# Kernel tuning notes

Measured on AMD Instinct MI355X. Metric: run time of the kernel, lower is better.

## Reference

```python
import jax, jax.numpy as jnp
import numpy as np
from jax.scipy.special import gammaln

L, R, W0, W1, B = 100, 3, 5, 20, 50


def mish(x):
    return x * jnp.tanh(jax.nn.softplus(x))


def conv1d(x, w, b):
    y = jax.lax.conv_general_dilated(x, w, (1,), 'VALID', dimension_numbers=('NCH', 'OIH', 'NCH'))
    return y + b[None, :, None]


def maxpool2(x):
    n = (x.shape[-1] // 2) * 2
    return x[..., :n].reshape(x.shape[0], x.shape[1], -1, 2).max(-1)


def dir_lp(x, alpha):
    # Dirichlet(alpha) log-prob over last dim, capped at 3.0 as in pwm_pr_lp/gamma_pr_lp
    K = x.shape[-1]
    lp = ((alpha - 1.0) * jnp.log(x)).sum(-1) + gammaln(K * alpha) - K * gammaln(alpha)
    return jnp.minimum(3.0, lp)


def binom_lp(n, k):
    # Binomial(n, 0.5) log pmf
    return gammaln(n + 1.0) - gammaln(k + 1.0) - gammaln(n - k + 1.0) + n * jnp.log(0.5)


def dlog_lp(a, b, mean, s, x):
    # DiscreteLogistic on [a,b]; log_prob evaluated at shifted value x (true value v = x + a)
    v = x + a
    up = jnp.where(v >= b, 1.0, jax.nn.sigmoid((v + 0.5 - mean) / s))
    lo = jnp.where(v <= a, 0.0, jax.nn.sigmoid((v - 0.5 - mean) / s))
    return jnp.log(up - lo + 1e-12)


def elbo(pwm_logits, wn_W1, wn_b1, wn_W2, wn_b2, wn_W3, wn_b3,
         gn_c1W, gn_c1b, gn_c2W, gn_c2b, gn_l1W, gn_l1b, gn_l2W, gn_l2b,
         zn_c1W, zn_c1b, zn_c2W, zn_c2b, zn_clsW, zn_clsb, zn_delW, zn_delb, X):
    pwm = jax.nn.softmax(pwm_logits, -1)              # [R,W1,4] PWM probabilities
    pwm_log = jnp.log(pwm)
    log_prior = dir_lp(pwm, 0.2).sum()
    # w guide net (Dropout inactive at eval)
    h = mish(wn_W1[0] + wn_b1)
    h = mish(h @ wn_W2 + wn_b2)
    ww = jax.nn.sigmoid(h @ wn_W3 + wn_b3)            # [R]
    mean = ww * (W1 - W0) + W0
    # cartesian product of floor/ceil per motif (torch.cartesian_prod: first var slowest)
    bits = (jnp.arange(8)[:, None] >> jnp.arange(2, -1, -1)[None, :]) & 1
    w2f = jnp.where(bits == 1, jnp.ceil(mean)[None, :], jnp.floor(mean)[None, :])  # [8,R]
    w_lp = dlog_lp(float(W0), float(W1), mean[None, :], 0.05, w2f - W0)            # [8,R]
    w_prob = jnp.exp(w_lp).T                                                        # [R,8]
    log_prior = log_prior + jnp.dot(w_prob.prod(0), binom_lp(float(W1 - W0), w2f).sum(1))
    log_guide = jnp.dot(w_prob.prod(0), w_lp.sum(1))
    # S[b,j,p,k] = log pwm[j,k,X[b,p+k]] -- replaces diag_embed + conv1d + log
    pidx = jnp.clip(jnp.arange(L)[:, None] + jnp.arange(W1)[None, :], 0, L - 1)
    Xoh = jax.nn.one_hot(X[:, pidx], 4, dtype=pwm.dtype)                            # [B,L,W1,4]
    S = jnp.einsum('bpkc,jkc->bjpk', Xoh, pwm_log)                                  # [B,R,L,W1]
    q = jnp.arange(L)
    kk = jnp.arange(W1)
    log_X = jnp.float32(0.0)
    for i_w in range(2 ** R):
        w = w2f[i_w].astype(jnp.int32)                                              # [R]
        kmask = (kk[None, :] < w[:, None]).astype(S.dtype)                          # [R,W1]
        ymid = (S * kmask[None, :, None, :]).sum(-1) / w.astype(S.dtype)[None, :, None]
        left = (w - 1) // 2
        valid = (q[None, :] >= left[:, None]) & (q[None, :] <= left[:, None] + (L - w)[:, None])
        src = jnp.clip(q[None, :] - left[:, None], 0, L - 1)
        ysh = jnp.take_along_axis(ymid, jnp.broadcast_to(src[None], ymid.shape), axis=2)
        y = jnp.where(valid[None], ysh, 0.0)                                        # [B,R,L]
        # gamma_net
        g = maxpool2(mish(conv1d(y, gn_c1W, gn_c1b)))
        g = maxpool2(mish(conv1d(g, gn_c2W, gn_c2b))).reshape(B, -1)                # [B,22]
        g = mish(g @ gn_l1W + gn_l1b)
        gamma = jax.nn.softmax(g @ gn_l2W + gn_l2b, -1)                             # [B,R]
        log_prior = log_prior + w_prob[:, i_w].prod() * dir_lp(gamma, 0.2).sum()
        for I in range(R):
            wI = w[I]
            I_pr = gamma[:, I]
            # z_net
            z = maxpool2(mish(conv1d(y[:, I:I + 1, :], zn_c1W, zn_c1b)))
            z = maxpool2(mish(conv1d(z, zn_c2W, zn_c2b))).reshape(B, -1)            # [B,176]
            Z_cls = z @ zn_clsW + zn_clsb                                           # [B,9]
            Z_del = jax.nn.sigmoid(z @ zn_delW + zn_delb)                           # [B,10]
            ind = jnp.argmax(Z_cls, 1) + 1
            gap = (99 - W1) / 10.0
            Z_m = (ind.astype(S.dtype) + Z_del[jnp.arange(B), ind]) * gap
            Z2 = jnp.stack([jnp.floor(Z_m), jnp.ceil(Z_m)], 0).astype(jnp.int32)    # [2,B]
            Z2f = Z2.astype(S.dtype)
            Z_lp = dlog_lp(0.0, 99.0, Z_m[None], 0.05, Z2f)
            Z_prob = jnp.exp(Z_lp)
            log_prior = log_prior + (w_prob[I, i_w] * Z_prob * I_pr[None] * binom_lp(float(L - W1 - 1), Z2f)).sum()
            log_guide = log_guide + (w_prob[I, i_w] * Z_prob * I_pr[None] * Z_lp).sum()
            # log_X: vectorized per-sample gather of pwm[I, k, X[i, Z+k]] for k < wI
            pos = jnp.clip(Z2[:, :, None] + kk[None, None, :], 0, L - 1)            # [2,B,W1]
            Xs = X[jnp.arange(B)[None, :, None], pos]                               # [2,B,W1]
            val = pwm_log[I][kk[None, None, :], Xs]                                 # [2,B,W1]
            lpv = (val * (kk[None, None, :] < wI)).sum(-1)                          # [2,B]
            log_X = log_X + w_prob[I, i_w] * (Z_prob * I_pr[None] * lpv).sum()
    return -log_X - log_prior + log_guide


def setup_inputs() -> dict:
    key = jax.random.key(0)
    ks = jax.random.split(key, 32)
    def n(i, shape, s=0.1):
        return (jax.random.normal(ks[i], shape) * s).astype(jnp.float32)
    return {
        'pwm_logits': n(0, (R, W1, 4), 0.5),
        'wn_W1': n(1, (1, 16)), 'wn_b1': n(2, (16,)),
        'wn_W2': n(3, (16, 16)), 'wn_b2': n(4, (16,)),
        'wn_W3': n(5, (16, 3), 0.01), 'wn_b3': n(6, (3,), 0.01),
        'gn_c1W': n(7, (16, 3, 5)), 'gn_c1b': n(8, (16,)),
        'gn_c2W': n(9, (1, 16, 5)), 'gn_c2b': n(10, (1,)),
        'gn_l1W': n(11, (22, 16)), 'gn_l1b': n(12, (16,)),
        'gn_l2W': n(13, (16, 3)), 'gn_l2b': n(14, (3,)),
        'zn_c1W': n(15, (16, 1, 5)), 'zn_c1b': n(16, (16,)),
        'zn_c2W': n(17, (8, 16, 5)), 'zn_c2b': n(18, (8,)),
        'zn_clsW': n(19, (176, 9)), 'zn_clsb': n(20, (9,)),
        'zn_delW': n(21, (176, 10)), 'zn_delb': n(22, (10,)),
        'X': jax.random.randint(ks[23], (B, L), 0, 4, dtype=jnp.int32),
    }


def reference(pwm_logits, wn_W1, wn_b1, wn_W2, wn_b2, wn_W3, wn_b3,
              gn_c1W, gn_c1b, gn_c2W, gn_c2b, gn_l1W, gn_l1b, gn_l2W, gn_l2b,
              zn_c1W, zn_c1b, zn_c2W, zn_c2b, zn_clsW, zn_clsb, zn_delW, zn_delb, X):
    return elbo(pwm_logits, wn_W1, wn_b1, wn_W2, wn_b2, wn_W3, wn_b3,
                gn_c1W, gn_c1b, gn_c2W, gn_c2b, gn_l1W, gn_l1b, gn_l2W, gn_l2b,
                zn_c1W, zn_c1b, zn_c2W, zn_c2b, zn_clsW, zn_clsb, zn_delW, zn_delb, X)
```

## Files before the change

kernel.cpp:

```cpp
#include <hip/hip_runtime.h>
#include <math.h>

#define LN2F 0.69314718055994530942f

#define WS_PWMLOG 0
#define WS_PJT    240
#define WS_WPROD  246
#define WS_BASEP  254
#define WS_BASEG  255
#define WS_WVF    256
#define WS_Y      272
#define WS_GAMMA  30272
#define WS_ZT     31472

__device__ __forceinline__ float sigm(float x){ return 1.0f/(1.0f+expf(-x)); }
__device__ __forceinline__ float mishf(float x){
    float sp = fmaxf(x,0.0f) + log1pf(expf(-fabsf(x)));
    return x * tanhf(sp);
}

__global__ void kA(const float* __restrict__ pwm_logits,
                   const float* __restrict__ wn_W1, const float* __restrict__ wn_b1,
                   const float* __restrict__ wn_W2, const float* __restrict__ wn_b2,
                   const float* __restrict__ wn_W3, const float* __restrict__ wn_b3,
                   float* __restrict__ ws)
{
    __shared__ float red[64];
    __shared__ float h1[16], h2s[16];
    int tid = threadIdx.x;
    float C4 = lgammaf(0.8f) - 4.0f*lgammaf(0.2f);
    float part = 0.0f;
    if (tid < 60) {
        const float* l = pwm_logits + tid*4;
        float m = fmaxf(fmaxf(l[0],l[1]),fmaxf(l[2],l[3]));
        float se = expf(l[0]-m)+expf(l[1]-m)+expf(l[2]-m)+expf(l[3]-m);
        float ls = logf(se);
        float dsum = 0.0f;
        for(int c=0;c<4;c++){ float pl = l[c]-m-ls; ws[WS_PWMLOG+tid*4+c]=pl; dsum+=pl; }
        float lp = -0.8f*dsum + C4;
        part = fminf(3.0f, lp);
    }
    red[tid]=part;
    __syncthreads();
    for(int s=32;s>0;s>>=1){ if(tid<s) red[tid]+=red[tid+s]; __syncthreads(); }

    if (tid<16) h1[tid] = mishf(wn_W1[tid]+wn_b1[tid]);
    __syncthreads();
    if (tid<16){
        float acc = wn_b2[tid];
        for(int i=0;i<16;i++) acc += h1[i]*wn_W2[i*16+tid];
        h2s[tid]=mishf(acc);
    }
    __syncthreads();
    if (tid==0){
        float mean[3];
        for(int o=0;o<3;o++){
            float acc=wn_b3[o];
            for(int i=0;i<16;i++) acc += h2s[i]*wn_W3[i*3+o];
            mean[o] = sigm(acc)*15.0f + 5.0f;
        }
        float pjt[3][2], wlp[3][2], bin[3][2];
        for(int j=0;j<3;j++){
            for(int t=0;t<2;t++){
                float wv = t ? ceilf(mean[j]) : floorf(mean[j]);
                float up = (wv>=20.0f)?1.0f:sigm((wv+0.5f-mean[j])/0.05f);
                float lo = (wv<=5.0f)?0.0f:sigm((wv-0.5f-mean[j])/0.05f);
                wlp[j][t] = logf(up-lo+1e-12f);
                pjt[j][t] = expf(wlp[j][t]);
                bin[j][t] = lgammaf(16.0f)-lgammaf(wv+1.0f)-lgammaf(16.0f-wv)+15.0f*(-LN2F);
                ws[WS_PJT+j*2+t]=pjt[j][t];
                ws[WS_WVF+j*2+t]=wv;
            }
        }
        float bp = red[0];
        float bg = 0.0f;
        for(int i=0;i<8;i++){
            int b0=(i>>2)&1, b1=(i>>1)&1, b2=i&1;
            float wp = pjt[0][b0]*pjt[1][b1]*pjt[2][b2];
            ws[WS_WPROD+i]=wp;
            bp += wp*(bin[0][b0]+bin[1][b1]+bin[2][b2]);
            bg += wp*(wlp[0][b0]+wlp[1][b1]+wlp[2][b2]);
        }
        ws[WS_BASEP]=bp;
        ws[WS_BASEG]=bg;
    }
}

__global__ void kB(const int* __restrict__ X, float* __restrict__ ws)
{
    int jt = blockIdx.x, b = blockIdx.y;
    int j = jt>>1;
    __shared__ int   xs[100];
    __shared__ float plj[80];
    int tid=threadIdx.x;
    if (tid<100) xs[tid]=X[b*100+tid];
    if (tid<80)  plj[tid]=ws[WS_PWMLOG+j*80+tid];
    __syncthreads();
    if (tid<100){
        int w = (int)ws[WS_WVF+jt];
        int left=(w-1)>>1;
        float yv=0.0f;
        if (tid>=left && tid<=left+100-w){
            int src=tid-left;
            float s=0.0f;
            for(int k=0;k<w;k++){
                int p=src+k; if(p>99)p=99;
                s+=plj[k*4+xs[p]];
            }
            yv=s/(float)w;
        }
        ws[WS_Y+(jt*50+b)*100+tid]=yv;
    }
}

__global__ void kC(const float* __restrict__ c1W, const float* __restrict__ c1b,
                   const float* __restrict__ c2W, const float* __restrict__ c2b,
                   const float* __restrict__ l1W, const float* __restrict__ l1b,
                   const float* __restrict__ l2W, const float* __restrict__ l2b,
                   float* __restrict__ ws)
{
    int iw=blockIdx.x, b=blockIdx.y, tid=threadIdx.x;
    __shared__ float yc[3][100];
    __shared__ float cw1[240];
    __shared__ float hp[16][48];
    __shared__ float c2o[44];
    __shared__ float g22[22];
    __shared__ float h16[16];
    for(int i=tid;i<300;i+=256){
        int j=i/100, q=i%100;
        int t=(iw>>(2-j))&1;
        yc[j][q]=ws[WS_Y+((j*2+t)*50+b)*100+q];
    }
    for(int i=tid;i<240;i+=256) cw1[i]=c1W[i];
    __syncthreads();
    for(int idx=tid; idx<768; idx+=256){
        int o=idx/48, p2=idx%48;
        float m=-1e30f;
        const float* wr=&cw1[o*15];
        for(int d=0;d<2;d++){
            int p=2*p2+d;
            float acc=c1b[o];
            for(int i=0;i<3;i++)
                for(int k=0;k<5;k++) acc += yc[i][p+k]*wr[i*5+k];
            m=fmaxf(m, mishf(acc));
        }
        hp[o][p2]=m;
    }
    __syncthreads();
    if (tid<44){
        float acc=c2b[0];
        for(int i=0;i<16;i++)
            for(int k=0;k<5;k++) acc+=hp[i][tid+k]*c2W[i*5+k];
        c2o[tid]=mishf(acc);
    }
    __syncthreads();
    if (tid<22) g22[tid]=fmaxf(c2o[2*tid],c2o[2*tid+1]);
    __syncthreads();
    if (tid<16){
        float acc=l1b[tid];
        for(int i=0;i<22;i++) acc+=g22[i]*l1W[i*16+tid];
        h16[tid]=mishf(acc);
    }
    __syncthreads();
    if (tid==0){
        float o3[3]; float m=-1e30f;
        for(int o=0;o<3;o++){
            float acc=l2b[o];
            for(int i=0;i<16;i++) acc+=h16[i]*l2W[i*3+o];
            o3[o]=acc; m=fmaxf(m,acc);
        }
        float se=0.0f; for(int o=0;o<3;o++){o3[o]=expf(o3[o]-m); se+=o3[o];}
        for(int o=0;o<3;o++) ws[WS_GAMMA+(iw*50+b)*3+o]=o3[o]/se;
    }
}

__global__ void kD(const int* __restrict__ X,
                   const float* __restrict__ c1W, const float* __restrict__ c1b,
                   const float* __restrict__ c2W, const float* __restrict__ c2b,
                   const float* __restrict__ clsW, const float* __restrict__ clsb,
                   const float* __restrict__ delW, const float* __restrict__ delb,
                   float* __restrict__ ws)
{
    int It=blockIdx.x, b=blockIdx.y, tid=threadIdx.x;
    int I=It>>1;
    __shared__ float y1[100];
    __shared__ int   xs[100];
    __shared__ float plI[80];
    __shared__ float zw1[80];
    __shared__ float zw2[640];
    __shared__ float hp[16][48];
    __shared__ float c2o[8][44];
    __shared__ float z[176];
    __shared__ float cls[9], del[10];
    if (tid<100){ y1[tid]=ws[WS_Y+(It*50+b)*100+tid]; xs[tid]=X[b*100+tid]; }
    if (tid>=128 && tid<208) { plI[tid-128]=ws[WS_PWMLOG+I*80+(tid-128)]; zw1[tid-128]=c1W[tid-128]; }
    for(int i=tid;i<640;i+=256) zw2[i]=c2W[i];
    __syncthreads();
    for(int idx=tid; idx<768; idx+=256){
        int o=idx/48, p2=idx%48;
        float m=-1e30f;
        for(int d=0;d<2;d++){
            int p=2*p2+d;
            float acc=c1b[o];
            for(int k=0;k<5;k++) acc+=y1[p+k]*zw1[o*5+k];
            m=fmaxf(m, mishf(acc));
        }
        hp[o][p2]=m;
    }
    __syncthreads();
    for(int idx=tid; idx<352; idx+=256){
        int o=idx/44, p=idx%44;
        float acc=c2b[o];
        for(int i=0;i<16;i++)
            for(int k=0;k<5;k++) acc+=hp[i][p+k]*zw2[(o*16+i)*5+k];
        c2o[o][p]=mishf(acc);
    }
    __syncthreads();
    if (tid<176){
        int o=tid/22, q=tid%22;
        z[tid]=fmaxf(c2o[o][2*q],c2o[o][2*q+1]);
    }
    __syncthreads();
    if (tid<9){
        float acc=clsb[tid];
        for(int m2=0;m2<176;m2++) acc+=z[m2]*clsW[m2*9+tid];
        cls[tid]=acc;
    }
    if (tid>=64 && tid<74){
        int n=tid-64;
        float acc=delb[n];
        for(int m2=0;m2<176;m2++) acc+=z[m2]*delW[m2*10+n];
        del[n]=sigm(acc);
    }
    __syncthreads();
    if (tid==0){
        int ind=0; float best=cls[0];
        for(int n=1;n<9;n++) if(cls[n]>best){best=cls[n];ind=n;}
        ind+=1;
        float Zm=((float)ind+del[ind])*7.9f;
        int wI=(int)ws[WS_WVF+It];
        float r0=0.0f,r1=0.0f,r2=0.0f;
        for(int s=0;s<2;s++){
            float zf = s? ceilf(Zm):floorf(Zm);
            float up = (zf>=99.0f)?1.0f:sigm((zf+0.5f-Zm)/0.05f);
            float lo = (zf<=0.0f)?0.0f:sigm((zf-0.5f-Zm)/0.05f);
            float zlp = logf(up-lo+1e-12f);
            float zp  = expf(zlp);
            float bin = lgammaf(80.0f)-lgammaf(zf+1.0f)-lgammaf(80.0f-zf)+79.0f*(-LN2F);
            int zi=(int)zf;
            float lpv=0.0f;
            for(int k=0;k<wI;k++){
                int p=zi+k; if(p<0)p=0; if(p>99)p=99;
                lpv+=plI[k*4+xs[p]];
            }
            r0+=zp*bin; r1+=zp*zlp; r2+=zp*lpv;
        }
        ws[WS_ZT+      It*50+b]=r0;
        ws[WS_ZT+300 + It*50+b]=r1;
        ws[WS_ZT+600 + It*50+b]=r2;
    }
}

__global__ void kE(const float* __restrict__ ws, float* __restrict__ out)
{
    int tid=threadIdx.x;
    __shared__ float sa[256], sb[256], sc[256];
    float C3 = lgammaf(0.6f) - 3.0f*lgammaf(0.2f);
    float pp=0.0f, pg=0.0f, px=0.0f;
    for(int idx=tid; idx<400; idx+=256){
        int iw=idx/50, b=idx%50;
        const float* g=&ws[WS_GAMMA+(iw*50+b)*3];
        float lp=-0.8f*(logf(g[0])+logf(g[1])+logf(g[2]))+C3;
        lp=fminf(3.0f,lp);
        pp += ws[WS_WPROD+iw]*lp;
    }
    for(int idx=tid; idx<300; idx+=256){
        int It=idx/50, b=idx%50;
        int I=It>>1, t=It&1;
        float gs=0.0f;
        for(int iw=0;iw<8;iw++)
            if(((iw>>(2-I))&1)==t) gs+=ws[WS_GAMMA+(iw*50+b)*3+I];
        float G=ws[WS_PJT+It]*gs;
        pp += G*ws[WS_ZT+idx];
        pg += G*ws[WS_ZT+300+idx];
        px += G*ws[WS_ZT+600+idx];
    }
    sa[tid]=pp; sb[tid]=pg; sc[tid]=px;
    __syncthreads();
    for(int s=128;s>0;s>>=1){
        if(tid<s){sa[tid]+=sa[tid+s];sb[tid]+=sb[tid+s];sc[tid]+=sc[tid+s];}
        __syncthreads();
    }
    if(tid==0){
        float log_prior=ws[WS_BASEP]+sa[0];
        float log_guide=ws[WS_BASEG]+sb[0];
        float log_X=sc[0];
        out[0] = -log_X - log_prior + log_guide;
    }
}

extern "C" void kernel_launch(void* const* d_in, const int* in_sizes, int n_in,
                              void* d_out, int out_size, void* d_ws, size_t ws_size,
                              hipStream_t stream)
{
    const float* pwm_logits=(const float*)d_in[0];
    const float* wn_W1 =(const float*)d_in[1];
    const float* wn_b1 =(const float*)d_in[2];
    const float* wn_W2 =(const float*)d_in[3];
    const float* wn_b2 =(const float*)d_in[4];
    const float* wn_W3 =(const float*)d_in[5];
    const float* wn_b3 =(const float*)d_in[6];
    const float* gn_c1W=(const float*)d_in[7];
    const float* gn_c1b=(const float*)d_in[8];
    const float* gn_c2W=(const float*)d_in[9];
    const float* gn_c2b=(const float*)d_in[10];
    const float* gn_l1W=(const float*)d_in[11];
    const float* gn_l1b=(const float*)d_in[12];
    const float* gn_l2W=(const float*)d_in[13];
    const float* gn_l2b=(const float*)d_in[14];
    const float* zn_c1W=(const float*)d_in[15];
    const float* zn_c1b=(const float*)d_in[16];
    const float* zn_c2W=(const float*)d_in[17];
    const float* zn_c2b=(const float*)d_in[18];
    const float* zn_clsW=(const float*)d_in[19];
    const float* zn_clsb=(const float*)d_in[20];
    const float* zn_delW=(const float*)d_in[21];
    const float* zn_delb=(const float*)d_in[22];
    const int*   X     =(const int*)d_in[23];
    float* ws =(float*)d_ws;
    float* out=(float*)d_out;

    hipLaunchKernelGGL(kA, dim3(1),      dim3(64),  0, stream,
                       pwm_logits, wn_W1, wn_b1, wn_W2, wn_b2, wn_W3, wn_b3, ws);
    hipLaunchKernelGGL(kB, dim3(6,50),   dim3(128), 0, stream, X, ws);
    hipLaunchKernelGGL(kC, dim3(8,50),   dim3(256), 0, stream,
                       gn_c1W, gn_c1b, gn_c2W, gn_c2b, gn_l1W, gn_l1b, gn_l2W, gn_l2b, ws);
    hipLaunchKernelGGL(kD, dim3(6,50),   dim3(256), 0, stream,
                       X, zn_c1W, zn_c1b, zn_c2W, zn_c2b, zn_clsW, zn_clsb, zn_delW, zn_delb, ws);
    hipLaunchKernelGGL(kE, dim3(1),      dim3(256), 0, stream, ws, out);
}
```

Measured before the change: 143.6 us.

## Fuse five kernels into two by recomputing small shared prelude per block

Merges the PWM/width-net, sliding-window score, gamma-net and z-net kernels into one 700-block kernel. Each block recomputes the PWM log-softmax, the width net and its own window-score rows in shared memory, and the finalize kernel recomputes the prior terms itself. This removes three launches and the global round trips through workspace, in exchange for redundant tiny computations in every block. Mish is also rewritten with a single exp and an algebraic tanh(softplus) form instead of log1p plus tanh.

```diff
diff --git a/kernel.cpp b/kernel.cpp
--- a/kernel.cpp
+++ b/kernel.cpp
@@ -3,276 +3,279 @@
 
 #define LN2F 0.69314718055994530942f
 
-#define WS_PWMLOG 0
-#define WS_PJT    240
-#define WS_WPROD  246
-#define WS_BASEP  254
-#define WS_BASEG  255
-#define WS_WVF    256
-#define WS_Y      272
-#define WS_GAMMA  30272
-#define WS_ZT     31472
+#define WS_GAMMA 0
+#define WS_ZT    1200
 
 __device__ __forceinline__ float sigm(float x){ return 1.0f/(1.0f+expf(-x)); }
 __device__ __forceinline__ float mishf(float x){
-    float sp = fmaxf(x,0.0f) + log1pf(expf(-fabsf(x)));
-    return x * tanhf(sp);
+    if (x >= 30.0f) return x;
+    float w = expf(x);
+    float u = 1.0f + w; u *= u;
+    return x * (u - 1.0f) / (u + 1.0f);
 }
 
-__global__ void kA(const float* __restrict__ pwm_logits,
-                   const float* __restrict__ wn_W1, const float* __restrict__ wn_b1,
-                   const float* __restrict__ wn_W2, const float* __restrict__ wn_b2,
-                   const float* __restrict__ wn_W3, const float* __restrict__ wn_b3,
-                   float* __restrict__ ws)
+__global__ __launch_bounds__(256) void kMain(
+    const float* __restrict__ pwm_logits,
+    const float* __restrict__ wn_W1, const float* __restrict__ wn_b1,
+    const float* __restrict__ wn_W2, const float* __restrict__ wn_b2,
+    const float* __restrict__ wn_W3, const float* __restrict__ wn_b3,
+    const float* __restrict__ gc1W, const float* __restrict__ gc1b,
+    const float* __restrict__ gc2W, const float* __restrict__ gc2b,
+    const float* __restrict__ gl1W, const float* __restrict__ gl1b,
+    const float* __restrict__ gl2W, const float* __restrict__ gl2b,
+    const float* __restrict__ zc1W, const float* __restrict__ zc1b,
+    const float* __restrict__ zc2W, const float* __restrict__ zc2b,
+    const float* __restrict__ zclsW, const float* __restrict__ zclsb,
+    const float* __restrict__ zdelW, const float* __restrict__ zdelb,
+    const int* __restrict__ X, float* __restrict__ ws)
 {
-    __shared__ float red[64];
-    __shared__ float h1[16], h2s[16];
-    int tid = threadIdx.x;
-    float C4 = lgammaf(0.8f) - 4.0f*lgammaf(0.2f);
-    float part = 0.0f;
-    if (tid < 60) {
-        const float* l = pwm_logits + tid*4;
-        float m = fmaxf(fmaxf(l[0],l[1]),fmaxf(l[2],l[3]));
-        float se = expf(l[0]-m)+expf(l[1]-m)+expf(l[2]-m)+expf(l[3]-m);
-        float ls = logf(se);
-        float dsum = 0.0f;
-        for(int c=0;c<4;c++){ float pl = l[c]-m-ls; ws[WS_PWMLOG+tid*4+c]=pl; dsum+=pl; }
-        float lp = -0.8f*dsum + C4;
-        part = fminf(3.0f, lp);
-    }
-    red[tid]=part;
-    __syncthreads();
-    for(int s=32;s>0;s>>=1){ if(tid<s) red[tid]+=red[tid+s]; __syncthreads(); }
-
-    if (tid<16) h1[tid] = mishf(wn_W1[tid]+wn_b1[tid]);
-    __syncthreads();
-    if (tid<16){
-        float acc = wn_b2[tid];
-        for(int i=0;i<16;i++) acc += h1[i]*wn_W2[i*16+tid];
-        h2s[tid]=mishf(acc);
-    }
-    __syncthreads();
-    if (tid==0){
-        float mean[3];
-        for(int o=0;o<3;o++){
-            float acc=wn_b3[o];
-            for(int i=0;i<16;i++) acc += h2s[i]*wn_W3[i*3+o];
-            mean[o] = sigm(acc)*15.0f + 5.0f;
-        }
-        float pjt[3][2], wlp[3][2], bin[3][2];
-        for(int j=0;j<3;j++){
-            for(int t=0;t<2;t++){
-                float wv = t ? ceilf(mean[j]) : floorf(mean[j]);
-                float up = (wv>=20.0f)?1.0f:sigm((wv+0.5f-mean[j])/0.05f);
-                float lo = (wv<=5.0f)?0.0f:sigm((wv-0.5f-mean[j])/0.05f);
-                wlp[j][t] = logf(up-lo+1e-12f);
-                pjt[j][t] = expf(wlp[j][t]);
-                bin[j][t] = lgammaf(16.0f)-lgammaf(wv+1.0f)-lgammaf(16.0f-wv)+15.0f*(-LN2F);
-                ws[WS_PJT+j*2+t]=pjt[j][t];
-                ws[WS_WVF+j*2+t]=wv;
-            }
-        }
-        float bp = red[0];
-        float bg = 0.0f;
-        for(int i=0;i<8;i++){
-            int b0=(i>>2)&1, b1=(i>>1)&1, b2=i&1;
-            float wp = pjt[0][b0]*pjt[1][b1]*pjt[2][b2];
-            ws[WS_WPROD+i]=wp;
-            bp += wp*(bin[0][b0]+bin[1][b1]+bin[2][b2]);
-            bg += wp*(wlp[0][b0]+wlp[1][b1]+wlp[2][b2]);
-        }
-        ws[WS_BASEP]=bp;
-        ws[WS_BASEG]=bg;
-    }
-}
-
-__global__ void kB(const int* __restrict__ X, float* __restrict__ ws)
-{
-    int jt = blockIdx.x, b = blockIdx.y;
-    int j = jt>>1;
+    int tid=threadIdx.x, bid=blockIdx.x;
+    bool isC = bid < 400;
+    int iw=0, b, It=0, I=0;
+    if(isC){ iw=bid%8; b=bid/8; }
+    else   { int idx=bid-400; It=idx%6; b=idx/6; I=It>>1; }
+
+    __shared__ float pl[240];
     __shared__ int   xs[100];
-    __shared__ float plj[80];
-    int tid=threadIdx.x;
-    if (tid<100) xs[tid]=X[b*100+tid];
-    if (tid<80)  plj[tid]=ws[WS_PWMLOG+j*80+tid];
-    __syncthreads();
-    if (tid<100){
-        int w = (int)ws[WS_WVF+jt];
-        int left=(w-1)>>1;
-        float yv=0.0f;
-        if (tid>=left && tid<=left+100-w){
-            int src=tid-left;
-            float s=0.0f;
-            for(int k=0;k<w;k++){
-                int p=src+k; if(p>99)p=99;
-                s+=plj[k*4+xs[p]];
-            }
-            yv=s/(float)w;
-        }
-        ws[WS_Y+(jt*50+b)*100+tid]=yv;
-    }
-}
-
-__global__ void kC(const float* __restrict__ c1W, const float* __restrict__ c1b,
-                   const float* __restrict__ c2W, const float* __restrict__ c2b,
-                   const float* __restrict__ l1W, const float* __restrict__ l1b,
-                   const float* __restrict__ l2W, const float* __restrict__ l2b,
-                   float* __restrict__ ws)
-{
-    int iw=blockIdx.x, b=blockIdx.y, tid=threadIdx.x;
-    __shared__ float yc[3][100];
-    __shared__ float cw1[240];
-    __shared__ float hp[16][48];
-    __shared__ float c2o[44];
-    __shared__ float g22[22];
-    __shared__ float h16[16];
-    for(int i=tid;i<300;i+=256){
-        int j=i/100, q=i%100;
-        int t=(iw>>(2-j))&1;
-        yc[j][q]=ws[WS_Y+((j*2+t)*50+b)*100+q];
-    }
-    for(int i=tid;i<240;i+=256) cw1[i]=c1W[i];
-    __syncthreads();
-    for(int idx=tid; idx<768; idx+=256){
-        int o=idx/48, p2=idx%48;
-        float m=-1e30f;
-        const float* wr=&cw1[o*15];
-        for(int d=0;d<2;d++){
-            int p=2*p2+d;
-            float acc=c1b[o];
-            for(int i=0;i<3;i++)
-                for(int k=0;k<5;k++) acc += yc[i][p+k]*wr[i*5+k];
-            m=fmaxf(m, mishf(acc));
-        }
-        hp[o][p2]=m;
-    }
-    __syncthreads();
-    if (tid<44){
-        float acc=c2b[0];
-        for(int i=0;i<16;i++)
-            for(int k=0;k<5;k++) acc+=hp[i][tid+k]*c2W[i*5+k];
-        c2o[tid]=mishf(acc);
-    }
-    __syncthreads();
-    if (tid<22) g22[tid]=fmaxf(c2o[2*tid],c2o[2*tid+1]);
-    __syncthreads();
-    if (tid<16){
-        float acc=l1b[tid];
-        for(int i=0;i<22;i++) acc+=g22[i]*l1W[i*16+tid];
-        h16[tid]=mishf(acc);
-    }
-    __syncthreads();
-    if (tid==0){
-        float o3[3]; float m=-1e30f;
-        for(int o=0;o<3;o++){
-            float acc=l2b[o];
-            for(int i=0;i<16;i++) acc+=h16[i]*l2W[i*3+o];
-            o3[o]=acc; m=fmaxf(m,acc);
-        }
-        float se=0.0f; for(int o=0;o<3;o++){o3[o]=expf(o3[o]-m); se+=o3[o];}
-        for(int o=0;o<3;o++) ws[WS_GAMMA+(iw*50+b)*3+o]=o3[o]/se;
-    }
-}
-
-__global__ void kD(const int* __restrict__ X,
-                   const float* __restrict__ c1W, const float* __restrict__ c1b,
-                   const float* __restrict__ c2W, const float* __restrict__ c2b,
-                   const float* __restrict__ clsW, const float* __restrict__ clsb,
-                   const float* __restrict__ delW, const float* __restrict__ delb,
-                   float* __restrict__ ws)
-{
-    int It=blockIdx.x, b=blockIdx.y, tid=threadIdx.x;
-    int I=It>>1;
-    __shared__ float y1[100];
-    __shared__ int   xs[100];
-    __shared__ float plI[80];
-    __shared__ float zw1[80];
+    __shared__ float h1[16], h2[16], wv6[6];
+    __shared__ float ybuf[3][100];
+    __shared__ float w1buf[240];
     __shared__ float zw2[640];
     __shared__ float hp[16][48];
     __shared__ float c2o[8][44];
-    __shared__ float z[176];
+    __shared__ float zz[176];
     __shared__ float cls[9], del[10];
-    if (tid<100){ y1[tid]=ws[WS_Y+(It*50+b)*100+tid]; xs[tid]=X[b*100+tid]; }
-    if (tid>=128 && tid<208) { plI[tid-128]=ws[WS_PWMLOG+I*80+(tid-128)]; zw1[tid-128]=c1W[tid-128]; }
-    for(int i=tid;i<640;i+=256) zw2[i]=c2W[i];
-    __syncthreads();
-    for(int idx=tid; idx<768; idx+=256){
-        int o=idx/48, p2=idx%48;
-        float m=-1e30f;
-        for(int d=0;d<2;d++){
-            int p=2*p2+d;
-            float acc=c1b[o];
-            for(int k=0;k<5;k++) acc+=y1[p+k]*zw1[o*5+k];
-            m=fmaxf(m, mishf(acc));
-        }
-        hp[o][p2]=m;
-    }
-    __syncthreads();
-    for(int idx=tid; idx<352; idx+=256){
-        int o=idx/44, p=idx%44;
-        float acc=c2b[o];
-        for(int i=0;i<16;i++)
-            for(int k=0;k<5;k++) acc+=hp[i][p+k]*zw2[(o*16+i)*5+k];
-        c2o[o][p]=mishf(acc);
-    }
-    __syncthreads();
-    if (tid<176){
-        int o=tid/22, q=tid%22;
-        z[tid]=fmaxf(c2o[o][2*q],c2o[o][2*q+1]);
-    }
-    __syncthreads();
-    if (tid<9){
-        float acc=clsb[tid];
-        for(int m2=0;m2<176;m2++) acc+=z[m2]*clsW[m2*9+tid];
-        cls[tid]=acc;
-    }
-    if (tid>=64 && tid<74){
-        int n=tid-64;
-        float acc=delb[n];
-        for(int m2=0;m2<176;m2++) acc+=z[m2]*delW[m2*10+n];
-        del[n]=sigm(acc);
-    }
-    __syncthreads();
-    if (tid==0){
-        int ind=0; float best=cls[0];
-        for(int n=1;n<9;n++) if(cls[n]>best){best=cls[n];ind=n;}
-        ind+=1;
-        float Zm=((float)ind+del[ind])*7.9f;
-        int wI=(int)ws[WS_WVF+It];
-        float r0=0.0f,r1=0.0f,r2=0.0f;
-        for(int s=0;s<2;s++){
-            float zf = s? ceilf(Zm):floorf(Zm);
-            float up = (zf>=99.0f)?1.0f:sigm((zf+0.5f-Zm)/0.05f);
-            float lo = (zf<=0.0f)?0.0f:sigm((zf-0.5f-Zm)/0.05f);
-            float zlp = logf(up-lo+1e-12f);
-            float zp  = expf(zlp);
-            float bin = lgammaf(80.0f)-lgammaf(zf+1.0f)-lgammaf(80.0f-zf)+79.0f*(-LN2F);
-            int zi=(int)zf;
-            float lpv=0.0f;
-            for(int k=0;k<wI;k++){
-                int p=zi+k; if(p<0)p=0; if(p>99)p=99;
-                lpv+=plI[k*4+xs[p]];
+    __shared__ float g22[22], h16[16];
+
+    if(tid<60){
+        const float* l=pwm_logits+tid*4;
+        float m=fmaxf(fmaxf(l[0],l[1]),fmaxf(l[2],l[3]));
+        float se=expf(l[0]-m)+expf(l[1]-m)+expf(l[2]-m)+expf(l[3]-m);
+        float ls=logf(se);
+        for(int c=0;c<4;c++) pl[tid*4+c]=l[c]-m-ls;
+    }
+    if(tid>=64 && tid<164) xs[tid-64]=X[b*100+tid-64];
+    if(tid>=192 && tid<208) h1[tid-192]=mishf(wn_W1[tid-192]+wn_b1[tid-192]);
+    __syncthreads();
+    if(tid<16){
+        float a=wn_b2[tid];
+        for(int i=0;i<16;i++) a+=h1[i]*wn_W2[i*16+tid];
+        h2[tid]=mishf(a);
+    }
+    __syncthreads();
+    if(tid<6){
+        int j=tid>>1;
+        float a=wn_b3[j];
+        for(int i=0;i<16;i++) a+=h2[i]*wn_W3[i*3+j];
+        float mean=sigm(a)*15.0f+5.0f;
+        wv6[tid]=(tid&1)?ceilf(mean):floorf(mean);
+    }
+    if(isC){ for(int i=tid;i<240;i+=256) w1buf[i]=gc1W[i]; }
+    else{
+        for(int i=tid;i<80;i+=256)  w1buf[i]=zc1W[i];
+        for(int i=tid;i<640;i+=256) zw2[i]=zc2W[i];
+    }
+    __syncthreads();
+
+    int np = isC ? 3 : 1;
+    for(int idx=tid; idx<np*100; idx+=256){
+        int jj=idx/100, q=idx%100;
+        int j = isC ? jj : I;
+        int t = isC ? ((iw>>(2-jj))&1) : (It&1);
+        int w=(int)wv6[j*2+t];
+        int left=(w-1)>>1;
+        float yv=0.0f;
+        if(q>=left && q<=left+100-w){
+            int src=q-left;
+            float s=0.0f;
+            const float* pj=&pl[j*80];
+            for(int k=0;k<w;k++) s+=pj[k*4+xs[src+k]];
+            yv=s/(float)w;
+        }
+        ybuf[jj][q]=yv;
+    }
+    __syncthreads();
+
+    if(isC){
+        for(int idx=tid; idx<768; idx+=256){
+            int o=idx/48, p2=idx%48;
+            const float* wr=&w1buf[o*15];
+            float bo=gc1b[o], m=-1e30f;
+            for(int d=0;d<2;d++){
+                int p=2*p2+d;
+                float acc=bo;
+                for(int i=0;i<3;i++)
+                    for(int k=0;k<5;k++) acc+=ybuf[i][p+k]*wr[i*5+k];
+                m=fmaxf(m,mishf(acc));
             }
-            r0+=zp*bin; r1+=zp*zlp; r2+=zp*lpv;
-        }
-        ws[WS_ZT+      It*50+b]=r0;
-        ws[WS_ZT+300 + It*50+b]=r1;
-        ws[WS_ZT+600 + It*50+b]=r2;
+            hp[o][p2]=m;
+        }
+        __syncthreads();
+        if(tid<44){
+            float acc=gc2b[0];
+            for(int i=0;i<16;i++)
+                for(int k=0;k<5;k++) acc+=hp[i][tid+k]*gc2W[i*5+k];
+            c2o[0][tid]=mishf(acc);
+        }
+        __syncthreads();
+        if(tid<22) g22[tid]=fmaxf(c2o[0][2*tid],c2o[0][2*tid+1]);
+        __syncthreads();
+        if(tid<16){
+            float acc=gl1b[tid];
+            for(int i=0;i<22;i++) acc+=g22[i]*gl1W[i*16+tid];
+            h16[tid]=mishf(acc);
+        }
+        __syncthreads();
+        if(tid==0){
+            float o3[3], m=-1e30f;
+            for(int o=0;o<3;o++){
+                float acc=gl2b[o];
+                for(int i=0;i<16;i++) acc+=h16[i]*gl2W[i*3+o];
+                o3[o]=acc; m=fmaxf(m,acc);
+            }
+            float se=0.0f;
+            for(int o=0;o<3;o++){ o3[o]=expf(o3[o]-m); se+=o3[o]; }
+            float inv=1.0f/se;
+            for(int o=0;o<3;o++) ws[WS_GAMMA+(iw*50+b)*3+o]=o3[o]*inv;
+        }
+    } else {
+        for(int idx=tid; idx<768; idx+=256){
+            int o=idx/48, p2=idx%48;
+            const float* wr=&w1buf[o*5];
+            float bo=zc1b[o], m=-1e30f;
+            for(int d=0;d<2;d++){
+                int p=2*p2+d;
+                float acc=bo;
+                for(int k=0;k<5;k++) acc+=ybuf[0][p+k]*wr[k];
+                m=fmaxf(m,mishf(acc));
+            }
+            hp[o][p2]=m;
+        }
+        __syncthreads();
+        for(int idx=tid; idx<352; idx+=256){
+            int o=idx/44, p=idx%44;
+            float acc=zc2b[o];
+            for(int i=0;i<16;i++)
+                for(int k=0;k<5;k++) acc+=hp[i][p+k]*zw2[(o*16+i)*5+k];
+            c2o[o][p]=mishf(acc);
+        }
+        __syncthreads();
+        if(tid<176){
+            int o=tid/22, q=tid%22;
+            zz[tid]=fmaxf(c2o[o][2*q],c2o[o][2*q+1]);
+        }
+        __syncthreads();
+        if(tid<9){
+            float acc=zclsb[tid];
+            for(int m2=0;m2<176;m2++) acc+=zz[m2]*zclsW[m2*9+tid];
+            cls[tid]=acc;
+        }
+        if(tid>=64 && tid<74){
+            int n=tid-64;
+            float acc=zdelb[n];
+            for(int m2=0;m2<176;m2++) acc+=zz[m2]*zdelW[m2*10+n];
+            del[n]=sigm(acc);
+        }
+        __syncthreads();
+        if(tid==0){
+            int ind=0; float best=cls[0];
+            for(int n=1;n<9;n++) if(cls[n]>best){best=cls[n];ind=n;}
+            ind+=1;
+            float Zm=((float)ind+del[ind])*7.9f;
+            int wI=(int)wv6[It];
+            float r0=0,r1=0,r2=0;
+            const float* pI=&pl[I*80];
+            for(int s=0;s<2;s++){
+                float zf=s?ceilf(Zm):floorf(Zm);
+                float up=(zf>=99.0f)?1.0f:sigm((zf+0.5f-Zm)*20.0f);
+                float lo=(zf<=0.0f)?0.0f:sigm((zf-0.5f-Zm)*20.0f);
+                float zlp=logf(up-lo+1e-12f);
+                float zp=expf(zlp);
+                float bin=lgammaf(80.0f)-lgammaf(zf+1.0f)-lgammaf(80.0f-zf)-79.0f*LN2F;
+                int zi=(int)zf;
+                float lpv=0.0f;
+                for(int k=0;k<wI;k++){
+                    int p=zi+k; if(p>99)p=99;
+                    lpv+=pI[k*4+xs[p]];
+                }
+                r0+=zp*bin; r1+=zp*zlp; r2+=zp*lpv;
+            }
+            ws[WS_ZT+    It*50+b]=r0;
+            ws[WS_ZT+300+It*50+b]=r1;
+            ws[WS_ZT+600+It*50+b]=r2;
+        }
     }
 }
 
-__global__ void kE(const float* __restrict__ ws, float* __restrict__ out)
+__global__ __launch_bounds__(256) void kFin(
+    const float* __restrict__ pwm_logits,
+    const float* __restrict__ wn_W1, const float* __restrict__ wn_b1,
+    const float* __restrict__ wn_W2, const float* __restrict__ wn_b2,
+    const float* __restrict__ wn_W3, const float* __restrict__ wn_b3,
+    const float* __restrict__ ws, float* __restrict__ out)
 {
+    __shared__ float sa[256], sb[256], sc[256];
+    __shared__ float h1[16], h2[16];
+    __shared__ float pjt[6], wlp6[6], bin6[6];
+    __shared__ float wprod[8];
+    __shared__ float bp_s, bg_s;
     int tid=threadIdx.x;
-    __shared__ float sa[256], sb[256], sc[256];
-    float C3 = lgammaf(0.6f) - 3.0f*lgammaf(0.2f);
+    float C4=lgammaf(0.8f)-4.0f*lgammaf(0.2f);
+    float C3=lgammaf(0.6f)-3.0f*lgammaf(0.2f);
+
+    float part=0.0f;
+    if(tid<60){
+        const float* l=pwm_logits+tid*4;
+        float m=fmaxf(fmaxf(l[0],l[1]),fmaxf(l[2],l[3]));
+        float se=expf(l[0]-m)+expf(l[1]-m)+expf(l[2]-m)+expf(l[3]-m);
+        float ls=logf(se);
+        float dsum=0.0f;
+        for(int c=0;c<4;c++) dsum+=l[c]-m-ls;
+        part=fminf(3.0f, -0.8f*dsum+C4);
+    }
+    sa[tid]=part;
+    if(tid<16) h1[tid]=mishf(wn_W1[tid]+wn_b1[tid]);
+    __syncthreads();
+    for(int s=128;s>0;s>>=1){ if(tid<s) sa[tid]+=sa[tid+s]; __syncthreads(); }
+    float dirsum = sa[0];
+    if(tid<16){
+        float a=wn_b2[tid];
+        for(int i=0;i<16;i++) a+=h1[i]*wn_W2[i*16+tid];
+        h2[tid]=mishf(a);
+    }
+    __syncthreads();
+    if(tid<6){
+        int j=tid>>1;
+        float a=wn_b3[j];
+        for(int i=0;i<16;i++) a+=h2[i]*wn_W3[i*3+j];
+        float mean=sigm(a)*15.0f+5.0f;
+        float wv=(tid&1)?ceilf(mean):floorf(mean);
+        float up=(wv>=20.0f)?1.0f:sigm((wv+0.5f-mean)*20.0f);
+        float lo=(wv<=5.0f)?0.0f:sigm((wv-0.5f-mean)*20.0f);
+        wlp6[tid]=logf(up-lo+1e-12f);
+        pjt[tid]=expf(wlp6[tid]);
+        bin6[tid]=lgammaf(16.0f)-lgammaf(wv+1.0f)-lgammaf(16.0f-wv)-15.0f*LN2F;
+    }
+    __syncthreads();
+    if(tid==0){
+        float bp=dirsum, bg=0.0f;
+        for(int i=0;i<8;i++){
+            int b0=(i>>2)&1, b1=(i>>1)&1, b2=i&1;
+            float wp=pjt[b0]*pjt[2+b1]*pjt[4+b2];
+            wprod[i]=wp;
+            bp+=wp*(bin6[b0]+bin6[2+b1]+bin6[4+b2]);
+            bg+=wp*(wlp6[b0]+wlp6[2+b1]+wlp6[4+b2]);
+        }
+        bp_s=bp; bg_s=bg;
+    }
+    __syncthreads();
+
     float pp=0.0f, pg=0.0f, px=0.0f;
     for(int idx=tid; idx<400; idx+=256){
         int iw=idx/50, b=idx%50;
         const float* g=&ws[WS_GAMMA+(iw*50+b)*3];
         float lp=-0.8f*(logf(g[0])+logf(g[1])+logf(g[2]))+C3;
-        lp=fminf(3.0f,lp);
-        pp += ws[WS_WPROD+iw]*lp;
+        pp += wprod[iw]*fminf(3.0f,lp);
     }
     for(int idx=tid; idx<300; idx+=256){
         int It=idx/50, b=idx%50;
@@ -280,7 +283,7 @@
         float gs=0.0f;
         for(int iw=0;iw<8;iw++)
             if(((iw>>(2-I))&1)==t) gs+=ws[WS_GAMMA+(iw*50+b)*3+I];
-        float G=ws[WS_PJT+It]*gs;
+        float G=pjt[It]*gs;
         pp += G*ws[WS_ZT+idx];
         pg += G*ws[WS_ZT+300+idx];
         px += G*ws[WS_ZT+600+idx];
@@ -288,14 +291,13 @@
     sa[tid]=pp; sb[tid]=pg; sc[tid]=px;
     __syncthreads();
     for(int s=128;s>0;s>>=1){
-        if(tid<s){sa[tid]+=sa[tid+s];sb[tid]+=sb[tid+s];sc[tid]+=sc[tid+s];}
+        if(tid<s){ sa[tid]+=sa[tid+s]; sb[tid]+=sb[tid+s]; sc[tid]+=sc[tid+s]; }
         __syncthreads();
     }
     if(tid==0){
-        float log_prior=ws[WS_BASEP]+sa[0];
-        float log_guide=ws[WS_BASEG]+sb[0];
-        float log_X=sc[0];
-        out[0] = -log_X - log_prior + log_guide;
+        float log_prior=bp_s+sa[0];
+        float log_guide=bg_s+sb[0];
+        out[0] = -sc[0] - log_prior + log_guide;
     }
 }
 
@@ -330,12 +332,11 @@
     float* ws =(float*)d_ws;
     float* out=(float*)d_out;
 
-    hipLaunchKernelGGL(kA, dim3(1),      dim3(64),  0, stream,
-                       pwm_logits, wn_W1, wn_b1, wn_W2, wn_b2, wn_W3, wn_b3, ws);
-    hipLaunchKernelGGL(kB, dim3(6,50),   dim3(128), 0, stream, X, ws);
-    hipLaunchKernelGGL(kC, dim3(8,50),   dim3(256), 0, stream,
-                       gn_c1W, gn_c1b, gn_c2W, gn_c2b, gn_l1W, gn_l1b, gn_l2W, gn_l2b, ws);
-    hipLaunchKernelGGL(kD, dim3(6,50),   dim3(256), 0, stream,
-                       X, zn_c1W, zn_c1b, zn_c2W, zn_c2b, zn_clsW, zn_clsb, zn_delW, zn_delb, ws);
-    hipLaunchKernelGGL(kE, dim3(1),      dim3(256), 0, stream, ws, out);
+    hipLaunchKernelGGL(kMain, dim3(700), dim3(256), 0, stream,
+                       pwm_logits, wn_W1, wn_b1, wn_W2, wn_b2, wn_W3, wn_b3,
+                       gn_c1W, gn_c1b, gn_c2W, gn_c2b, gn_l1W, gn_l1b, gn_l2W, gn_l2b,
+                       zn_c1W, zn_c1b, zn_c2W, zn_c2b, zn_clsW, zn_clsb, zn_delW, zn_delb,
+                       X, ws);
+    hipLaunchKernelGGL(kFin, dim3(1),   dim3(256), 0, stream,
+                       pwm_logits, wn_W1, wn_b1, wn_W2, wn_b2, wn_W3, wn_b3, ws, out);
 }
```

Measured after the change: 124.3 us. -13.5%, faster.
